# Optimization experiments

Measured on AMD Instinct MI355X. Metric: run time of the kernel, lower is better.

The kernel has to match this reference:

```python
import jax, jax.numpy as jnp
import numpy as np

TAG_THR = 0.1
MIN_HEIGHT = 0.0
PULL_WEIGHT = 1.0
PUSH_WEIGHT = 1.0
EPS = 1e-6


def _bbox_iou(boxes):
    # boxes: [N,4] -> IoU [N,N] (standard, no +1 offset; heights in the loss
    # are also computed without +1)
    x1, y1, x2, y2 = boxes[:, 0], boxes[:, 1], boxes[:, 2], boxes[:, 3]
    area = (x2 - x1) * (y2 - y1)
    iw = jnp.clip(jnp.minimum(x2[:, None], x2[None, :]) - jnp.maximum(x1[:, None], x1[None, :]), 0.0)
    ih = jnp.clip(jnp.minimum(y2[:, None], y2[None, :]) - jnp.maximum(y1[:, None], y1[None, :]), 0.0)
    inter = iw * ih
    union = area[:, None] + area[None, :] - inter
    return inter / jnp.maximum(union, 1e-12)


def _single_image(pred, gt_inds, proposals):
    # pred [N,D], gt_inds [N] int, proposals [N,5]
    N = pred.shape[0]
    heights = proposals[:, 3] - proposals[:, 1]
    valid = (gt_inds >= 0) & (heights > MIN_HEIGHT)
    scores = proposals[:, 4]
    iou = _bbox_iou(proposals[:, :4])  # [N,N]

    def step(state, _):
        alive, tot_pull, tot_push, pull_cnt, push_cnt = state
        active = jnp.sum(alive) >= 2  # pop i; if nothing remains, the torch loop breaks
        # i = highest-scoring remaining proposal (greedy, score-sorted)
        i = jnp.argmax(jnp.where(alive, scores, -jnp.inf))
        rem = alive.at[i].set(False)
        overlap = (iou[i] > 0.0) & rem
        diff = jnp.mean((pred - pred[i]) ** 2, axis=1)  # [N]
        check = diff < TAG_THR
        same = gt_inds == gt_inds[i]
        pull_m = overlap & same & ~check
        push_m = overlap & ~same & check
        pn = jnp.sum(pull_m)
        qn = jnp.sum(push_m)
        pull_l = jnp.sum(jnp.where(pull_m, diff * scores, 0.0)) / jnp.maximum(pn, 1).astype(diff.dtype)
        push_l = jnp.sum(jnp.where(push_m, jnp.exp(-diff) * scores, 0.0)) / jnp.maximum(qn, 1).astype(diff.dtype)
        add_pull = active & (pn > 0)
        add_push = active & (qn > 0)
        tot_pull = tot_pull + jnp.where(add_pull, pull_l, 0.0)
        tot_push = tot_push + jnp.where(add_push, push_l, 0.0)
        pull_cnt = pull_cnt + add_pull.astype(jnp.float32)
        push_cnt = push_cnt + add_push.astype(jnp.float32)
        # suppress everything overlapping i whose tag is already close (diff < thr)
        new_alive = rem & ~(overlap & check)
        alive = jnp.where(active, new_alive, alive)
        return (alive, tot_pull, tot_push, pull_cnt, push_cnt), None

    z = jnp.float32(0.0)
    init = (valid, z, z, z, z)
    (_, tot_pull, tot_push, pull_cnt, push_cnt), _ = jax.lax.scan(step, init, None, length=N)
    pull = tot_pull / (pull_cnt + EPS)
    push = tot_push / (push_cnt + EPS)
    return push, pull


def setup_inputs() -> dict:
    key = jax.random.key(0)
    k1, k2, k3, k4, k5, k6, k7 = jax.random.split(key, 7)
    IMGS, N, D = 4, 2000, 4
    pred = jax.random.normal(k1, (IMGS, N, D), dtype=jnp.float32)
    gt_inds = jax.random.randint(k2, (IMGS, N), 0, 50, dtype=jnp.int32)
    x1 = jax.random.uniform(k3, (IMGS, N), minval=0.0, maxval=800.0)
    y1 = jax.random.uniform(k4, (IMGS, N), minval=0.0, maxval=800.0)
    w = jax.random.uniform(k5, (IMGS, N), minval=8.0, maxval=128.0)
    h = jax.random.uniform(k6, (IMGS, N), minval=8.0, maxval=128.0)
    score = jax.random.uniform(k7, (IMGS, N), minval=0.0, maxval=1.0)
    proposals = jnp.stack([x1, y1, x1 + w, y1 + h, score], axis=-1).astype(jnp.float32)
    gt_bboxes = jax.random.uniform(jax.random.fold_in(key, 9), (IMGS, 20, 4), dtype=jnp.float32)
    return {"pred": pred, "gt_inds": gt_inds, "proposals": proposals, "gt_bboxes": gt_bboxes}


def reference(pred, gt_inds, proposals, gt_bboxes):
    # gt_bboxes is accepted by the torch forward but never used in the loss math.
    push, pull = jax.vmap(_single_image)(pred, gt_inds, proposals)  # per-image scalars
    img_num = pred.shape[0]
    push_loss = jnp.sum(push) / img_num * PUSH_WEIGHT
    pull_loss = jnp.sum(pull) / img_num * PULL_WEIGHT
    return push_loss, pull_loss
```

## Files before the change

kernel.cpp:

```cpp
#include <hip/hip_runtime.h>
#include <stdint.h>

#define BLOCK 256
#define KMAX 8
#define NWAVES (BLOCK / 64)
#define S2 2048
#define NW 32
#define NCH 32
#define SPB 16
#define PB (S2 / SPB)
#define RB (S2 / BLOCK)
#define PCAP 65536
#define LDSP2 4096
#define BCAP 64
#define EFF_INF 0x7FFFFFFF

__device__ inline int rank_of(const unsigned long long* ss, int j) {
    int jw = j >> 6, jb = j & 63;
    int rk = __popcll(ss[jw] & (jb ? (~0ull >> (64 - jb)) : 0ull));
    for (int w = 0; w < jw; ++w) rk += __popcll(ss[w]);
    return rk;
}

__global__ __launch_bounds__(BLOCK) void rankcount_kernel(
    const float* __restrict__ proposals,
    int* __restrict__ partial, int* __restrict__ pcnt, int N, int imgs)
{
    const int bi = blockIdx.x, bj = blockIdx.y, img = blockIdx.z;
    const int t = threadIdx.x;
    if (bi == 0 && bj == 0 && t == 0) pcnt[img] = 0;
    const float* P = proposals + (size_t)img * N * 5;
    __shared__ unsigned sj[BLOCK];
    const int jbase = bj * BLOCK;
    {
        int j = jbase + t;
        sj[t] = (j < N) ? __float_as_uint(P[j*5 + 4]) : 0u;
    }
    __syncthreads();
    const int i = bi * BLOCK + t;
    if (i >= N) return;
    const unsigned my = __float_as_uint(P[i*5 + 4]);
    int p = 0;
    const uint4* s4 = (const uint4*)sj;
#pragma unroll
    for (int q = 0; q < BLOCK/4; ++q) {
        uint4 v = s4[q];
        int jj = jbase + q*4;
        p += (int)((v.x > my) | ((v.x == my) & (jj + 0 < i)));
        p += (int)((v.y > my) | ((v.y == my) & (jj + 1 < i)));
        p += (int)((v.z > my) | ((v.z == my) & (jj + 2 < i)));
        p += (int)((v.w > my) | ((v.w == my) & (jj + 3 < i)));
    }
    partial[((size_t)(img*RB + bj))*S2 + i] = p;
}

__global__ __launch_bounds__(BLOCK) void rankscatter_kernel(
    const float* __restrict__ pred, const int* __restrict__ gt_inds,
    const float* __restrict__ proposals, const int* __restrict__ partial,
    float* __restrict__ soa, int* __restrict__ sgt, int N, int imgs)
{
    const int img = blockIdx.y, t = threadIdx.x;
    const int i = blockIdx.x * BLOCK + t;
    const size_t stride = (size_t)imgs * S2;
    const size_t base   = (size_t)img * S2;

    if (i >= N) {
        if (i < S2) {
#pragma unroll
            for (int a = 0; a < 9; ++a) soa[(size_t)a*stride + base + i] = 0.f;
            sgt[base + i] = -1;
        }
        return;
    }

    const float* P = proposals + (size_t)img * N * 5;
    const float* E = pred      + (size_t)img * N * 4;
    const int*   G = gt_inds   + (size_t)img * N;

    const float p0 = P[i*5+0], p1 = P[i*5+1], p2 = P[i*5+2],
                p3 = P[i*5+3], p4 = P[i*5+4];
    const float q0 = E[i*4+0], q1 = E[i*4+1], q2 = E[i*4+2], q3 = E[i*4+3];
    const int   gg = G[i];

    int p = 0;
#pragma unroll
    for (int b = 0; b < RB; ++b)
        p += partial[((size_t)(img*RB + b))*S2 + i];

    soa[0*stride + base + p] = p0;
    soa[1*stride + base + p] = p1;
    soa[2*stride + base + p] = p2;
    soa[3*stride + base + p] = p3;
    soa[4*stride + base + p] = p4;
    soa[5*stride + base + p] = q0;
    soa[6*stride + base + p] = q1;
    soa[7*stride + base + p] = q2;
    soa[8*stride + base + p] = q3;
    sgt[base + p] = gg;
}

__global__ __launch_bounds__(BLOCK) void suppairs_kernel(
    const float* __restrict__ soa, unsigned* __restrict__ pairs,
    int* __restrict__ pcnt, int N, int imgs)
{
    const int ic = blockIdx.x, jc = blockIdx.y, img = blockIdx.z;
    if (ic < jc) return;
    const int t = threadIdx.x, wave = t >> 6, lane = t & 63;
    const size_t stride = (size_t)imgs * S2, base = (size_t)img * S2;
    __shared__ float si[8][64];
    for (int idx = t; idx < 512; idx += BLOCK) {
        int f = idx >> 6, e = idx & 63;
        int a = (f < 4) ? f : f + 1;
        si[f][e] = soa[(size_t)a*stride + base + ic*64 + e];
    }
    __syncthreads();
    const int j = jc*64 + lane;
    const float jx1 = soa[0*stride+base+j], jy1 = soa[1*stride+base+j];
    const float jx2 = soa[2*stride+base+j], jy2 = soa[3*stride+base+j];
    const float j0  = soa[5*stride+base+j], j1  = soa[6*stride+base+j];
    const float j2  = soa[7*stride+base+j], j3  = soa[8*stride+base+j];
    const bool jin = (j < N);
    unsigned* PL = pairs + (size_t)img * PCAP;
    for (int ii = 0; ii < 16; ++ii) {
        int il = wave*16 + ii;
        int i  = ic*64 + il;
        float bx1 = si[0][il], by1 = si[1][il], bx2 = si[2][il], by2 = si[3][il];
        float f0  = si[4][il], f1  = si[5][il], f2  = si[6][il], f3  = si[7][il];
        bool s = false;
        if (jin && i < N && i > j) {
            float iw = fminf(jx2, bx2) - fmaxf(jx1, bx1);
            float ih = fminf(jy2, by2) - fmaxf(jy1, by1);
            if (iw > 0.f && ih > 0.f) {
                float d0 = j0-f0, d1 = j1-f1, d2 = j2-f2, d3 = j3-f3;
                float diff = 0.25f*(d0*d0 + d1*d1 + d2*d2 + d3*d3);
                s = diff < 0.1f;
            }
        }
        unsigned long long m = __ballot(s);
        if (m) {
            int leader = __ffsll((unsigned long long)m) - 1;
            int basei = 0;
            if (lane == leader) basei = atomicAdd(&pcnt[img], __popcll(m));
            basei = __shfl(basei, leader);
            if (s) {
                int idx = basei + __popcll(m & ((lane == 0) ? 0ull : (~0ull >> (64 - lane))));
                if (idx < PCAP) PL[idx] = ((unsigned)j << 11) | (unsigned)i;
            }
        }
    }
}

__global__ __launch_bounds__(64) void greedy_kernel(
    const unsigned* __restrict__ pairs, const int* __restrict__ pcnt,
    const int* __restrict__ sgt, const float* __restrict__ soa,
    unsigned long long* __restrict__ selw_out, int imgs)
{
    const int img = blockIdx.x, l = threadIdx.x;
    const size_t stride = (size_t)imgs * S2, base = (size_t)img * S2;
    __shared__ unsigned long long slocAll[S2];
    __shared__ unsigned spair[LDSP2];
    __shared__ unsigned bucket[NCH * BCAP];
    __shared__ int bcnt[NCH];
    __shared__ unsigned long long skilled[NW], ssel[NW];

    int P = pcnt[img]; if (P > PCAP) P = PCAP;
    const unsigned* PL = pairs + (size_t)img * PCAP;
    const bool staged = (P <= LDSP2);

    for (int x = l; x < S2; x += 64) slocAll[x] = 0ull;
    if (l < NCH) bcnt[l] = 0;
    if (staged) for (int p = l; p < P; p += 64) spair[p] = PL[p];

    for (int c = 0; c < NCH; ++c) {
        const int j = c*64 + l;
        int g = sgt[base + j];
        float a = soa[1*stride + base + j];
        float b = soa[3*stride + base + j];
        bool invalid = !(g >= 0 && (b - a) > 0.f);
        unsigned long long bb = __ballot(invalid);
        if (l == 0) skilled[c] = bb;
    }
    __syncthreads();

    for (int p = l; p < P; p += 64) {
        unsigned v = staged ? spair[p] : PL[p];
        int lo = v >> 11, hi = v & 2047;
        if ((lo >> 6) == (hi >> 6)) {
            atomicOr(&slocAll[hi], 1ull << (lo & 63));
        } else {
            int idx = atomicAdd(&bcnt[lo >> 6], 1);
            if (idx < BCAP) bucket[(lo >> 6)*BCAP + idx] = v;
        }
    }
    __syncthreads();

    const unsigned long long lowmask = (l == 0) ? 0ull : (~0ull >> (64 - l));

    for (int c = 0; c < NCH; ++c) {
        unsigned long long U = ~skilled[c];
        const unsigned long long loc = slocAll[c*64 + l];
        unsigned long long sel = 0ull;
        while (U) {
            bool inU = (U >> l) & 1ull;
            unsigned long long A = __ballot(inU && ((loc & U & lowmask) == 0ull));
            sel |= A;
            bool kill = inU && !((A >> l) & 1ull) && ((loc & A) != 0ull);
            unsigned long long K = __ballot(kill);
            U &= ~(A | K);
        }
        if (l == 0) ssel[c] = sel;
        if (sel != 0ull) {
            const int bc = bcnt[c];
            if (bc <= BCAP) {
                for (int q = l; q < bc; q += 64) {
                    unsigned v = bucket[c*BCAP + q];
                    int lo = v >> 11, hi = v & 2047;
                    if ((sel >> (lo & 63)) & 1ull)
                        atomicOr(&skilled[hi >> 6], 1ull << (hi & 63));
                }
            } else {
                for (int p = l; p < P; p += 64) {
                    unsigned v = PL[p];
                    int lo = v >> 11, hi = v & 2047;
                    if ((lo >> 6) == c && (hi >> 6) != c &&
                        ((sel >> (lo & 63)) & 1ull))
                        atomicOr(&skilled[hi >> 6], 1ull << (hi & 63));
                }
            }
        }
        __syncthreads();
    }
    if (l < NW) selw_out[(size_t)img*NW + l] = ssel[l];
}

__global__ __launch_bounds__(BLOCK) void effsteps_kernel(
    const unsigned* __restrict__ pairs, const int* __restrict__ pcnt,
    const unsigned long long* __restrict__ selw,
    const int* __restrict__ sgt, const float* __restrict__ soa,
    int* __restrict__ eff, int* __restrict__ nsteps, int imgs)
{
    const int img = blockIdx.x, t = threadIdx.x;
    const int lane = t & 63, wave = t >> 6;
    const size_t stride = (size_t)imgs * S2, base = (size_t)img * S2;
    __shared__ unsigned long long ss[NW];
    __shared__ int sistar[S2];
    __shared__ unsigned hist[S2];
    __shared__ int ints[2*NWAVES];
    __shared__ unsigned wsum[NWAVES];
    __shared__ int bm[NWAVES];
    if (t < NW) ss[t] = selw[(size_t)img*NW + t];
    for (int x = t; x < S2; x += BLOCK) { sistar[x] = EFF_INF; hist[x] = 0u; }
    __syncthreads();

    int P = pcnt[img]; if (P > PCAP) P = PCAP;
    const unsigned* PL = pairs + (size_t)img * PCAP;
    for (int p = t; p < P; p += BLOCK) {
        unsigned v = PL[p];
        int lo = v >> 11, hi = v & 2047;
        if ((ss[lo >> 6] >> (lo & 63)) & 1ull) atomicMin(&sistar[hi], lo);
    }
    __syncthreads();

    int myV = 0, mySc = 0;
#pragma unroll
    for (int k = 0; k < 8; ++k) {
        const int j = k*BLOCK + t;
        int g = sgt[base + j];
        float a = soa[1*stride+base+j], b = soa[3*stride+base+j];
        bool valid = (g >= 0) && ((b - a) > 0.f);
        bool selb  = (ss[j>>6] >> (j & 63)) & 1ull;
        int e;
        if (!valid) e = 0;
        else if (selb) { e = rank_of(ss, j); ++myV; ++mySc; }
        else {
            ++myV;
            int istar = sistar[j];
            if (istar == EFF_INF) e = EFF_INF;
            else { e = rank_of(ss, istar) + 1; atomicAdd(&hist[e - 1], 1u); }
        }
        eff[(size_t)img*S2 + j] = e;
    }
    __syncthreads();

    int v = myV, sc = mySc;
    for (int o = 32; o > 0; o >>= 1) { v += __shfl_down(v, o); sc += __shfl_down(sc, o); }
    if (lane == 0) { ints[wave] = v; ints[NWAVES + wave] = sc; }
    __syncthreads();
    int V = 0, Sc = 0;
    for (int w = 0; w < NWAVES; ++w) { V += ints[w]; Sc += ints[NWAVES + w]; }

    unsigned loc[8]; unsigned s = 0;
#pragma unroll
    for (int k = 0; k < 8; ++k) { s += hist[t*8 + k]; loc[k] = s; }
    unsigned tot = s;
    for (int o = 1; o < 64; o <<= 1) {
        unsigned u = __shfl_up(tot, o);
        if (lane >= o) tot += u;
    }
    if (lane == 63) wsum[wave] = tot;
    __syncthreads();
    unsigned woff = 0;
    for (int w = 0; w < wave; ++w) woff += wsum[w];
    unsigned exclP = woff + tot - s;
    __syncthreads();
#pragma unroll
    for (int k = 0; k < 8; ++k) hist[t*8 + k] = exclP + loc[k];
    __syncthreads();

    int best = EFF_INF;
    for (int r = t; r < Sc; r += BLOCK) {
        unsigned rem = (r == 0) ? 0u : hist[r - 1];
        int alive = V - r - (int)rem;
        if (alive < 2) best = min(best, r);
    }
    for (int o = 32; o > 0; o >>= 1) best = min(best, __shfl_down(best, o));
    if (lane == 0) bm[wave] = best;
    __syncthreads();
    if (t == 0) {
        int b = bm[0];
        for (int w = 1; w < NWAVES; ++w) b = min(b, bm[w]);
        nsteps[img] = min(b, Sc);
    }
}

__global__ __launch_bounds__(BLOCK) void pairs_kernel(
    const float* __restrict__ soa, const int* __restrict__ sgt,
    const int* __restrict__ eff, const unsigned long long* __restrict__ selw,
    const int* __restrict__ nsteps, float* __restrict__ partials, int imgs)
{
    const int ic = blockIdx.x, img = blockIdx.y;
    const int t = threadIdx.x, wave = t >> 6, lane = t & 63;
    const size_t stride = (size_t)imgs * S2, base = (size_t)img * S2;
    __shared__ unsigned long long ss[NW];
    __shared__ float pw[NWAVES][4];
    __shared__ int anyact;
    if (t < NW) ss[t] = selw[(size_t)img*NW + t];
    if (t == 0) anyact = 0;
    __syncthreads();
    const int ns = nsteps[img];

    float bx1[4], by1[4], bx2[4], by2[4], f0[4], f1[4], f2[4], f3[4];
    int bgt[4], rk[4]; bool act[4];
    bool any = false;
#pragma unroll
    for (int u = 0; u < 4; ++u) {
        const int i = ic*SPB + wave*4 + u;
        bool selb = (ss[i>>6] >> (i & 63)) & 1ull;
        int r = rank_of(ss, i);
        rk[u] = r;
        act[u] = selb && (r < ns);
        any |= act[u];
        if (act[u]) {
            bx1[u] = soa[0*stride+base+i]; by1[u] = soa[1*stride+base+i];
            bx2[u] = soa[2*stride+base+i]; by2[u] = soa[3*stride+base+i];
            f0[u]  = soa[5*stride+base+i]; f1[u]  = soa[6*stride+base+i];
            f2[u]  = soa[7*stride+base+i]; f3[u]  = soa[8*stride+base+i];
            bgt[u] = sgt[base + i];
        } else {
            bx1[u]=by1[u]=bx2[u]=by2[u]=0.f; f0[u]=f1[u]=f2[u]=f3[u]=0.f; bgt[u]=-2;
        }
    }
    if (any && lane == 0) anyact = 1;
    __syncthreads();
    if (!anyact) {
        if (t < 4) partials[((size_t)img*PB + ic)*4 + t] = 0.f;
        return;
    }

    float ps[4] = {0,0,0,0}, pn[4] = {0,0,0,0}, qs[4] = {0,0,0,0}, qn[4] = {0,0,0,0};
    for (int jt = 0; jt < NCH; ++jt) {
        const int j = jt*64 + lane;
        const float jx1 = soa[0*stride+base+j], jy1 = soa[1*stride+base+j];
        const float jx2 = soa[2*stride+base+j], jy2 = soa[3*stride+base+j];
        const float jsc = soa[4*stride+base+j];
        const float j0  = soa[5*stride+base+j], j1  = soa[6*stride+base+j];
        const float j2  = soa[7*stride+base+j], j3  = soa[8*stride+base+j];
        const int   jgt = sgt[base + j];
        const int   jef = eff[(size_t)img*S2 + j];
#pragma unroll
        for (int u = 0; u < 4; ++u) {
            if (!act[u]) continue;
            if (rk[u] < jef) {
                float iw = fminf(jx2, bx2[u]) - fmaxf(jx1, bx1[u]);
                float ih = fminf(jy2, by2[u]) - fmaxf(jy1, by1[u]);
                if (iw > 0.f && ih > 0.f) {
                    float d0 = j0 - f0[u], d1 = j1 - f1[u];
                    float d2 = j2 - f2[u], d3 = j3 - f3[u];
                    float diff = 0.25f*(d0*d0 + d1*d1 + d2*d2 + d3*d3);
                    bool check = diff < 0.1f;
                    bool same  = (jgt == bgt[u]);
                    if (same && !check)      { ps[u] += diff * jsc;       pn[u] += 1.f; }
                    else if (!same && check) { qs[u] += expf(-diff)*jsc;  qn[u] += 1.f; }
                }
            }
        }
    }

    float sPull = 0.f, cPull = 0.f, sPush = 0.f, cPush = 0.f;
#pragma unroll
    for (int u = 0; u < 4; ++u) {
        if (!act[u]) continue;
        float a0 = ps[u], a1 = pn[u], a2 = qs[u], a3 = qn[u];
        for (int o = 32; o > 0; o >>= 1) {
            a0 += __shfl_down(a0, o); a1 += __shfl_down(a1, o);
            a2 += __shfl_down(a2, o); a3 += __shfl_down(a3, o);
        }
        if (lane == 0) {
            if (a1 > 0.f) { sPull += a0 / a1; cPull += 1.f; }
            if (a3 > 0.f) { sPush += a2 / a3; cPush += 1.f; }
        }
    }
    if (lane == 0) {
        pw[wave][0] = sPull; pw[wave][1] = cPull;
        pw[wave][2] = sPush; pw[wave][3] = cPush;
    }
    __syncthreads();
    if (t == 0) {
        float a = 0, b = 0, c = 0, d = 0;
        for (int w = 0; w < NWAVES; ++w) {
            a += pw[w][0]; b += pw[w][1]; c += pw[w][2]; d += pw[w][3];
        }
        float* p = partials + ((size_t)img*PB + ic)*4;
        p[0] = a; p[1] = b; p[2] = c; p[3] = d;
    }
}

__global__ __launch_bounds__(BLOCK) void finalize_kernel(
    const float* __restrict__ partials, float* __restrict__ out, int imgs)
{
    const int t = threadIdx.x;
    __shared__ float a[8][4];
    if (t < 32) ((float*)a)[t] = 0.f;
    __syncthreads();
    for (int e = t; e < imgs * PB; e += BLOCK) {
        int img = e / PB;
        const float* p = partials + (size_t)e * 4;
#pragma unroll
        for (int k = 0; k < 4; ++k) {
            float v = p[k];
            if (v != 0.f) atomicAdd(&a[img][k], v);
        }
    }
    __syncthreads();
    if (t == 0) {
        float push = 0.f, pull = 0.f;
        for (int i = 0; i < imgs; ++i) {
            pull += a[i][0] / (a[i][1] + 1e-6f);
            push += a[i][2] / (a[i][3] + 1e-6f);
        }
        out[0] = push / (float)imgs;
        out[1] = pull / (float)imgs;
    }
}

__global__ __launch_bounds__(BLOCK) void tagloss_kernel(
    const float* __restrict__ pred, const int* __restrict__ gt_inds,
    const float* __restrict__ proposals, float* __restrict__ ws, int N)
{
    const int img = blockIdx.x, t = threadIdx.x;
    const int lane = t & 63, wav = t >> 6;
    const float* P = proposals + (size_t)img * N * 5;
    const float* E = pred      + (size_t)img * N * 4;
    const int*   G = gt_inds   + (size_t)img * N;
    float x1[KMAX], y1[KMAX], x2[KMAX], y2[KMAX], sc[KMAX];
    float e0[KMAX], e1[KMAX], e2[KMAX], e3[KMAX];
    int gt[KMAX]; unsigned amask = 0u; int local_alive = 0;
#pragma unroll
    for (int k = 0; k < KMAX; ++k) {
        int j = k * BLOCK + t;
        if (j < N) {
            x1[k]=P[j*5+0]; y1[k]=P[j*5+1]; x2[k]=P[j*5+2]; y2[k]=P[j*5+3]; sc[k]=P[j*5+4];
            e0[k]=E[j*4+0]; e1[k]=E[j*4+1]; e2[k]=E[j*4+2]; e3[k]=E[j*4+3]; gt[k]=G[j];
            if (gt[k] >= 0 && (y2[k]-y1[k]) > 0.0f) { amask |= 1u<<k; local_alive++; }
        } else { x1[k]=y1[k]=x2[k]=y2[k]=0.f; sc[k]=0.f; e0[k]=e1[k]=e2[k]=e3[k]=0.f; gt[k]=-1; }
    }
    __shared__ unsigned long long s_key[NWAVES];
    __shared__ float s_b[9];
    __shared__ float s_part[NWAVES][5];
    int alive_count;
    {
        float v = (float)local_alive;
#pragma unroll
        for (int o = 32; o > 0; o >>= 1) v += __shfl_down(v, o);
        if (lane == 0) s_part[wav][0] = v;
        __syncthreads();
        float tot = 0.f;
        for (int w = 0; w < NWAVES; ++w) tot += s_part[w][0];
        alive_count = (int)tot;
    }
    float tot_pull=0.f, tot_push=0.f, pull_cnt=0.f, push_cnt=0.f;
    while (alive_count >= 2) {
        unsigned long long key = 0ull;
#pragma unroll
        for (int k = 0; k < KMAX; ++k)
            if (amask & (1u<<k)) {
                unsigned long long kk = ((unsigned long long)__float_as_uint(sc[k])<<32)
                                      | (unsigned long long)(0xFFFFFFFFu - (unsigned)(k*BLOCK+t));
                if (kk > key) key = kk;
            }
#pragma unroll
        for (int o = 32; o > 0; o >>= 1) {
            unsigned long long ok = __shfl_down(key, o);
            if (ok > key) key = ok;
        }
        if (lane == 0) s_key[wav] = key;
        __syncthreads();
        unsigned long long bk = s_key[0];
        for (int w = 1; w < NWAVES; ++w) if (s_key[w] > bk) bk = s_key[w];
        const int i = (int)(0xFFFFFFFFu - (unsigned)(bk & 0xFFFFFFFFull));
        if ((i & (BLOCK-1)) == t) {
            int k = i / BLOCK;
            s_b[0]=x1[k]; s_b[1]=y1[k]; s_b[2]=x2[k]; s_b[3]=y2[k];
            s_b[4]=e0[k]; s_b[5]=e1[k]; s_b[6]=e2[k]; s_b[7]=e3[k];
            s_b[8]=__int_as_float(gt[k]);
        }
        __syncthreads();
        const float bx1=s_b[0], by1=s_b[1], bx2=s_b[2], by2=s_b[3];
        const float f0=s_b[4], f1=s_b[5], f2=s_b[6], f3=s_b[7];
        const int bgt = __float_as_int(s_b[8]);
        const float areai = (bx2-bx1)*(by2-by1);
        float psum=0.f,qsum=0.f,pn=0.f,qn=0.f,scnt=0.f;
#pragma unroll
        for (int k = 0; k < KMAX; ++k) {
            if (!(amask & (1u<<k))) continue;
            int j = k*BLOCK+t;
            if (j == i) { amask &= ~(1u<<k); continue; }
            float iw = fmaxf(fminf(x2[k],bx2)-fmaxf(x1[k],bx1),0.f);
            float ih = fmaxf(fminf(y2[k],by2)-fmaxf(y1[k],by1),0.f);
            float inter = iw*ih;
            float uni = (x2[k]-x1[k])*(y2[k]-y1[k]) + areai - inter;
            float iou = inter / fmaxf(uni, 1e-12f);
            if (iou > 0.f) {
                float d0=e0[k]-f0,d1=e1[k]-f1,d2=e2[k]-f2,d3=e3[k]-f3;
                float diff = 0.25f*(d0*d0+d1*d1+d2*d2+d3*d3);
                bool check = diff < 0.1f;
                bool same = (gt[k]==bgt);
                if (same && !check) { psum += diff*sc[k]; pn += 1.f; }
                if (!same && check) { qsum += __expf(-diff)*sc[k]; qn += 1.f; }
                if (check)          { amask &= ~(1u<<k); scnt += 1.f; }
            }
        }
        float r0=psum,r1=pn,r2=qsum,r3=qn,r4=scnt;
#pragma unroll
        for (int o = 32; o > 0; o >>= 1) {
            r0+=__shfl_down(r0,o); r1+=__shfl_down(r1,o); r2+=__shfl_down(r2,o);
            r3+=__shfl_down(r3,o); r4+=__shfl_down(r4,o);
        }
        if (lane == 0) { s_part[wav][0]=r0;s_part[wav][1]=r1;s_part[wav][2]=r2;s_part[wav][3]=r3;s_part[wav][4]=r4; }
        __syncthreads();
        float T0=0,T1=0,T2=0,T3=0,T4=0;
        for (int w = 0; w < NWAVES; ++w) {
            T0+=s_part[w][0];T1+=s_part[w][1];T2+=s_part[w][2];T3+=s_part[w][3];T4+=s_part[w][4];
        }
        if (T1 > 0.f) { tot_pull += T0/T1; pull_cnt += 1.f; }
        if (T3 > 0.f) { tot_push += T2/T3; push_cnt += 1.f; }
        alive_count -= 1 + (int)T4;
    }
    if (t == 0) {
        ws[img*2+0] = tot_push / (push_cnt + 1e-6f);
        ws[img*2+1] = tot_pull / (pull_cnt + 1e-6f);
    }
}

__global__ void finalize_fb_kernel(const float* __restrict__ ws,
                                   float* __restrict__ out, int imgs)
{
    if (threadIdx.x == 0 && blockIdx.x == 0) {
        float push = 0.f, pull = 0.f;
        for (int k = 0; k < imgs; ++k) { push += ws[2*k]; pull += ws[2*k+1]; }
        out[0] = push / (float)imgs;
        out[1] = pull / (float)imgs;
    }
}

extern "C" void kernel_launch(void* const* d_in, const int* in_sizes, int n_in,
                              void* d_out, int out_size, void* d_ws, size_t ws_size,
                              hipStream_t stream) {
    const float* pred      = (const float*)d_in[0];
    const int*   gt_inds   = (const int*)  d_in[1];
    const float* proposals = (const float*)d_in[2];
    const int imgs = in_sizes[3] / 80;
    const int N    = in_sizes[1] / imgs;

    size_t off = 0;
    auto alloc = [&](size_t b) { size_t o = off; off += (b + 255) & ~(size_t)255; return o; };
    const size_t soa_off  = alloc((size_t)9 * imgs * S2 * 4);
    const size_t sgt_off  = alloc((size_t)imgs * S2 * 4);
    const size_t sel_off  = alloc((size_t)imgs * NW * 8);
    const size_t eff_off  = alloc((size_t)imgs * S2 * 4);
    const size_t nst_off  = alloc((size_t)imgs * 4);
    const size_t par_off  = alloc((size_t)imgs * PB * 16);
    const size_t rnk_off  = alloc((size_t)imgs * RB * S2 * 4);
    const size_t prs_off  = alloc((size_t)imgs * PCAP * 4);
    const size_t pcn_off  = alloc((size_t)imgs * 4);
    const size_t need = off;

    if (N <= S2 && imgs <= 8 && ws_size >= need) {
        char* w = (char*)d_ws;
        float*              soa  = (float*)(w + soa_off);
        int*                sgt  = (int*)(w + sgt_off);
        unsigned long long* sel  = (unsigned long long*)(w + sel_off);
        int*                eff  = (int*)(w + eff_off);
        int*                nst  = (int*)(w + nst_off);
        float*              par  = (float*)(w + par_off);
        int*                rnk  = (int*)(w + rnk_off);
        unsigned*           prs  = (unsigned*)(w + prs_off);
        int*                pcn  = (int*)(w + pcn_off);

        rankcount_kernel<<<dim3(RB, RB, imgs), BLOCK, 0, stream>>>(
            proposals, rnk, pcn, N, imgs);
        rankscatter_kernel<<<dim3(RB, imgs), BLOCK, 0, stream>>>(
            pred, gt_inds, proposals, rnk, soa, sgt, N, imgs);
        suppairs_kernel<<<dim3(NCH, NCH, imgs), BLOCK, 0, stream>>>(
            soa, prs, pcn, N, imgs);
        greedy_kernel<<<imgs, 64, 0, stream>>>(prs, pcn, sgt, soa, sel, imgs);
        effsteps_kernel<<<imgs, BLOCK, 0, stream>>>(prs, pcn, sel, sgt, soa,
                                                    eff, nst, imgs);
        pairs_kernel<<<dim3(PB, imgs), BLOCK, 0, stream>>>(soa, sgt, eff, sel,
                                                           nst, par, imgs);
        finalize_kernel<<<1, BLOCK, 0, stream>>>(par, (float*)d_out, imgs);
    } else {
        float* ws = (float*)d_ws;
        tagloss_kernel<<<imgs, BLOCK, 0, stream>>>(pred, gt_inds, proposals, ws, N);
        finalize_fb_kernel<<<1, 64, 0, stream>>>(ws, (float*)d_out, imgs);
    }
}
```

Measured before the change: 152.1 us.

## Fuse greedy with effsteps and pairs with finalize to cut kernel launches

```diff
diff --git a/kernel.cpp b/kernel.cpp
--- a/kernel.cpp
+++ b/kernel.cpp
@@ -15,20 +15,18 @@
 #define BCAP 64
 #define EFF_INF 0x7FFFFFFF
 
-__device__ inline int rank_of(const unsigned long long* ss, int j) {
-    int jw = j >> 6, jb = j & 63;
-    int rk = __popcll(ss[jw] & (jb ? (~0ull >> (64 - jb)) : 0ull));
-    for (int w = 0; w < jw; ++w) rk += __popcll(ss[w]);
-    return rk;
-}
-
 __global__ __launch_bounds__(BLOCK) void rankcount_kernel(
     const float* __restrict__ proposals,
-    int* __restrict__ partial, int* __restrict__ pcnt, int N, int imgs)
+    int* __restrict__ partial, int* __restrict__ pcnt,
+    float* __restrict__ acc, int* __restrict__ done, int N, int imgs)
 {
     const int bi = blockIdx.x, bj = blockIdx.y, img = blockIdx.z;
     const int t = threadIdx.x;
-    if (bi == 0 && bj == 0 && t == 0) pcnt[img] = 0;
+    if (bi == 0 && bj == 0 && img == 0) {
+        if (t < imgs) pcnt[t] = 0;
+        if (t >= 64 && t < 64 + imgs*4) acc[t - 64] = 0.f;
+        if (t == 128) *done = 0;
+    }
     const float* P = proposals + (size_t)img * N * 5;
     __shared__ unsigned sj[BLOCK];
     const int jbase = bj * BLOCK;
@@ -124,14 +122,13 @@
     for (int ii = 0; ii < 16; ++ii) {
         int il = wave*16 + ii;
         int i  = ic*64 + il;
-        float bx1 = si[0][il], by1 = si[1][il], bx2 = si[2][il], by2 = si[3][il];
-        float f0  = si[4][il], f1  = si[5][il], f2  = si[6][il], f3  = si[7][il];
         bool s = false;
         if (jin && i < N && i > j) {
-            float iw = fminf(jx2, bx2) - fmaxf(jx1, bx1);
-            float ih = fminf(jy2, by2) - fmaxf(jy1, by1);
+            float iw = fminf(jx2, si[2][il]) - fmaxf(jx1, si[0][il]);
+            float ih = fminf(jy2, si[3][il]) - fmaxf(jy1, si[1][il]);
             if (iw > 0.f && ih > 0.f) {
-                float d0 = j0-f0, d1 = j1-f1, d2 = j2-f2, d3 = j3-f3;
+                float d0 = j0-si[4][il], d1 = j1-si[5][il];
+                float d2 = j2-si[6][il], d3 = j3-si[7][il];
                 float diff = 0.25f*(d0*d0 + d1*d1 + d2*d2 + d3*d3);
                 s = diff < 0.1f;
             }
@@ -150,39 +147,52 @@
     }
 }
 
-__global__ __launch_bounds__(64) void greedy_kernel(
+__global__ __launch_bounds__(BLOCK) void greedyeff_kernel(
     const unsigned* __restrict__ pairs, const int* __restrict__ pcnt,
     const int* __restrict__ sgt, const float* __restrict__ soa,
-    unsigned long long* __restrict__ selw_out, int imgs)
+    unsigned long long* __restrict__ selw, int* __restrict__ eff,
+    int* __restrict__ nsteps, int imgs)
 {
-    const int img = blockIdx.x, l = threadIdx.x;
+    const int img = blockIdx.x, t = threadIdx.x;
+    const int lane = t & 63, wave = t >> 6;
     const size_t stride = (size_t)imgs * S2, base = (size_t)img * S2;
-    __shared__ unsigned long long slocAll[S2];
+
+    __shared__ __align__(16) char A[16384];
     __shared__ unsigned spair[LDSP2];
     __shared__ unsigned bucket[NCH * BCAP];
     __shared__ int bcnt[NCH];
-    __shared__ unsigned long long skilled[NW], ssel[NW];
+    __shared__ unsigned long long skilled[NW], ssel[NW], svalid[NW];
+    __shared__ int pfx[NW + 1];
+    __shared__ unsigned wsum[NWAVES];
+    __shared__ int bm[NWAVES];
+    __shared__ int sV;
+
+    unsigned long long* slocAll = (unsigned long long*)A;
 
     int P = pcnt[img]; if (P > PCAP) P = PCAP;
     const unsigned* PL = pairs + (size_t)img * PCAP;
     const bool staged = (P <= LDSP2);
 
-    for (int x = l; x < S2; x += 64) slocAll[x] = 0ull;
-    if (l < NCH) bcnt[l] = 0;
-    if (staged) for (int p = l; p < P; p += 64) spair[p] = PL[p];
-
-    for (int c = 0; c < NCH; ++c) {
-        const int j = c*64 + l;
-        int g = sgt[base + j];
+    for (int x = t; x < S2; x += BLOCK) slocAll[x] = 0ull;
+    if (t < NCH) bcnt[t] = 0;
+    if (t == 0) sV = 0;
+    __syncthreads();
+    if (staged) for (int p = t; p < P; p += BLOCK) spair[p] = PL[p];
+    for (int g = wave; g < NCH; g += NWAVES) {
+        int j = g*64 + lane;
+        int gv = sgt[base + j];
         float a = soa[1*stride + base + j];
         float b = soa[3*stride + base + j];
-        bool invalid = !(g >= 0 && (b - a) > 0.f);
+        bool invalid = !(gv >= 0 && (b - a) > 0.f);
         unsigned long long bb = __ballot(invalid);
-        if (l == 0) skilled[c] = bb;
-    }
-    __syncthreads();
-
-    for (int p = l; p < P; p += 64) {
+        if (lane == 0) {
+            skilled[g] = bb;
+            svalid[g] = ~bb;
+            atomicAdd(&sV, 64 - __popcll(bb));
+        }
+    }
+    __syncthreads();
+    for (int p = t; p < P; p += BLOCK) {
         unsigned v = staged ? spair[p] : PL[p];
         int lo = v >> 11, hi = v & 2047;
         if ((lo >> 6) == (hi >> 6)) {
@@ -194,104 +204,87 @@
     }
     __syncthreads();
 
-    const unsigned long long lowmask = (l == 0) ? 0ull : (~0ull >> (64 - l));
-
-    for (int c = 0; c < NCH; ++c) {
-        unsigned long long U = ~skilled[c];
-        const unsigned long long loc = slocAll[c*64 + l];
-        unsigned long long sel = 0ull;
-        while (U) {
-            bool inU = (U >> l) & 1ull;
-            unsigned long long A = __ballot(inU && ((loc & U & lowmask) == 0ull));
-            sel |= A;
-            bool kill = inU && !((A >> l) & 1ull) && ((loc & A) != 0ull);
-            unsigned long long K = __ballot(kill);
-            U &= ~(A | K);
-        }
-        if (l == 0) ssel[c] = sel;
-        if (sel != 0ull) {
-            const int bc = bcnt[c];
-            if (bc <= BCAP) {
-                for (int q = l; q < bc; q += 64) {
-                    unsigned v = bucket[c*BCAP + q];
-                    int lo = v >> 11, hi = v & 2047;
-                    if ((sel >> (lo & 63)) & 1ull)
-                        atomicOr(&skilled[hi >> 6], 1ull << (hi & 63));
+    if (wave == 0) {
+        const unsigned long long lowmask = (lane == 0) ? 0ull : (~0ull >> (64 - lane));
+        for (int c = 0; c < NCH; ++c) {
+            unsigned long long U = ~skilled[c];
+            const unsigned long long loc = slocAll[c*64 + lane];
+            unsigned long long sel = 0ull;
+            while (U) {
+                bool inU = (U >> lane) & 1ull;
+                unsigned long long Am = __ballot(inU && ((loc & U & lowmask) == 0ull));
+                sel |= Am;
+                bool kill = inU && !((Am >> lane) & 1ull) && ((loc & Am) != 0ull);
+                unsigned long long K = __ballot(kill);
+                U &= ~(Am | K);
+            }
+            if (lane == 0) ssel[c] = sel;
+            if (sel != 0ull) {
+                const int bc = bcnt[c];
+                if (bc <= BCAP) {
+                    for (int q = lane; q < bc; q += 64) {
+                        unsigned v = bucket[c*BCAP + q];
+                        int lo = v >> 11, hi = v & 2047;
+                        if ((sel >> (lo & 63)) & 1ull)
+                            atomicOr(&skilled[hi >> 6], 1ull << (hi & 63));
+                    }
+                } else {
+                    for (int p = lane; p < P; p += 64) {
+                        unsigned v = PL[p];
+                        int lo = v >> 11, hi = v & 2047;
+                        if ((lo >> 6) == c && (hi >> 6) != c &&
+                            ((sel >> (lo & 63)) & 1ull))
+                            atomicOr(&skilled[hi >> 6], 1ull << (hi & 63));
+                    }
                 }
-            } else {
-                for (int p = l; p < P; p += 64) {
-                    unsigned v = PL[p];
-                    int lo = v >> 11, hi = v & 2047;
-                    if ((lo >> 6) == c && (hi >> 6) != c &&
-                        ((sel >> (lo & 63)) & 1ull))
-                        atomicOr(&skilled[hi >> 6], 1ull << (hi & 63));
-                }
-            }
-        }
-        __syncthreads();
-    }
-    if (l < NW) selw_out[(size_t)img*NW + l] = ssel[l];
-}
-
-__global__ __launch_bounds__(BLOCK) void effsteps_kernel(
-    const unsigned* __restrict__ pairs, const int* __restrict__ pcnt,
-    const unsigned long long* __restrict__ selw,
-    const int* __restrict__ sgt, const float* __restrict__ soa,
-    int* __restrict__ eff, int* __restrict__ nsteps, int imgs)
-{
-    const int img = blockIdx.x, t = threadIdx.x;
-    const int lane = t & 63, wave = t >> 6;
-    const size_t stride = (size_t)imgs * S2, base = (size_t)img * S2;
-    __shared__ unsigned long long ss[NW];
-    __shared__ int sistar[S2];
-    __shared__ unsigned hist[S2];
-    __shared__ int ints[2*NWAVES];
-    __shared__ unsigned wsum[NWAVES];
-    __shared__ int bm[NWAVES];
-    if (t < NW) ss[t] = selw[(size_t)img*NW + t];
+            }
+        }
+    }
+    __syncthreads();
+    if (t < NW) selw[(size_t)img*NW + t] = ssel[t];
+
+    int* sistar = (int*)A;
+    unsigned* hist = (unsigned*)(A + 8192);
     for (int x = t; x < S2; x += BLOCK) { sistar[x] = EFF_INF; hist[x] = 0u; }
-    __syncthreads();
-
-    int P = pcnt[img]; if (P > PCAP) P = PCAP;
-    const unsigned* PL = pairs + (size_t)img * PCAP;
+    if (t == 0) {
+        int s = 0;
+        for (int w = 0; w < NW; ++w) { pfx[w] = s; s += __popcll(ssel[w]); }
+        pfx[NW] = s;
+    }
+    __syncthreads();
     for (int p = t; p < P; p += BLOCK) {
-        unsigned v = PL[p];
+        unsigned v = staged ? spair[p] : PL[p];
         int lo = v >> 11, hi = v & 2047;
-        if ((ss[lo >> 6] >> (lo & 63)) & 1ull) atomicMin(&sistar[hi], lo);
-    }
-    __syncthreads();
-
-    int myV = 0, mySc = 0;
+        if ((ssel[lo >> 6] >> (lo & 63)) & 1ull) atomicMin(&sistar[hi], lo);
+    }
+    __syncthreads();
 #pragma unroll
     for (int k = 0; k < 8; ++k) {
         const int j = k*BLOCK + t;
-        int g = sgt[base + j];
-        float a = soa[1*stride+base+j], b = soa[3*stride+base+j];
-        bool valid = (g >= 0) && ((b - a) > 0.f);
-        bool selb  = (ss[j>>6] >> (j & 63)) & 1ull;
+        const int jw = j >> 6, jb = j & 63;
+        bool valid = (svalid[jw] >> jb) & 1ull;
+        bool selb  = (ssel[jw] >> jb) & 1ull;
         int e;
         if (!valid) e = 0;
-        else if (selb) { e = rank_of(ss, j); ++myV; ++mySc; }
+        else if (selb)
+            e = pfx[jw] + __popcll(ssel[jw] & (jb ? (~0ull >> (64 - jb)) : 0ull));
         else {
-            ++myV;
-            int istar = sistar[j];
-            if (istar == EFF_INF) e = EFF_INF;
-            else { e = rank_of(ss, istar) + 1; atomicAdd(&hist[e - 1], 1u); }
+            int is = sistar[j];
+            if (is == EFF_INF) e = EFF_INF;
+            else {
+                int iw_ = is >> 6, ib = is & 63;
+                e = pfx[iw_] + __popcll(ssel[iw_] & (ib ? (~0ull >> (64 - ib)) : 0ull)) + 1;
+                atomicAdd(&hist[e - 1], 1u);
+            }
         }
         eff[(size_t)img*S2 + j] = e;
     }
     __syncthreads();
 
-    int v = myV, sc = mySc;
-    for (int o = 32; o > 0; o >>= 1) { v += __shfl_down(v, o); sc += __shfl_down(sc, o); }
-    if (lane == 0) { ints[wave] = v; ints[NWAVES + wave] = sc; }
-    __syncthreads();
-    int V = 0, Sc = 0;
-    for (int w = 0; w < NWAVES; ++w) { V += ints[w]; Sc += ints[NWAVES + w]; }
-
-    unsigned loc[8]; unsigned s = 0;
-#pragma unroll
-    for (int k = 0; k < 8; ++k) { s += hist[t*8 + k]; loc[k] = s; }
+    const int V = sV, Sc = pfx[NW];
+    unsigned loc8[8]; unsigned s = 0;
+#pragma unroll
+    for (int k = 0; k < 8; ++k) { s += hist[t*8 + k]; loc8[k] = s; }
     unsigned tot = s;
     for (int o = 1; o < 64; o <<= 1) {
         unsigned u = __shfl_up(tot, o);
@@ -304,9 +297,8 @@
     unsigned exclP = woff + tot - s;
     __syncthreads();
 #pragma unroll
-    for (int k = 0; k < 8; ++k) hist[t*8 + k] = exclP + loc[k];
-    __syncthreads();
-
+    for (int k = 0; k < 8; ++k) hist[t*8 + k] = exclP + loc8[k];
+    __syncthreads();
     int best = EFF_INF;
     for (int r = t; r < Sc; r += BLOCK) {
         unsigned rem = (r == 0) ? 0u : hist[r - 1];
@@ -323,17 +315,18 @@
     }
 }
 
-__global__ __launch_bounds__(BLOCK) void pairs_kernel(
+__global__ __launch_bounds__(BLOCK) void pairsfinal_kernel(
     const float* __restrict__ soa, const int* __restrict__ sgt,
     const int* __restrict__ eff, const unsigned long long* __restrict__ selw,
-    const int* __restrict__ nsteps, float* __restrict__ partials, int imgs)
+    const int* __restrict__ nsteps, float* __restrict__ acc,
+    int* __restrict__ done, float* __restrict__ out, int imgs)
 {
     const int ic = blockIdx.x, img = blockIdx.y;
     const int t = threadIdx.x, wave = t >> 6, lane = t & 63;
     const size_t stride = (size_t)imgs * S2, base = (size_t)img * S2;
     __shared__ unsigned long long ss[NW];
     __shared__ float pw[NWAVES][4];
-    __shared__ int anyact;
+    __shared__ int anyact, ticket;
     if (t < NW) ss[t] = selw[(size_t)img*NW + t];
     if (t == 0) anyact = 0;
     __syncthreads();
@@ -345,8 +338,10 @@
 #pragma unroll
     for (int u = 0; u < 4; ++u) {
         const int i = ic*SPB + wave*4 + u;
-        bool selb = (ss[i>>6] >> (i & 63)) & 1ull;
-        int r = rank_of(ss, i);
+        const int iw_ = i >> 6, ib = i & 63;
+        bool selb = (ss[iw_] >> ib) & 1ull;
+        int r = __popcll(ss[iw_] & (ib ? (~0ull >> (64 - ib)) : 0ull));
+        for (int w = 0; w < iw_; ++w) r += __popcll(ss[w]);
         rk[u] = r;
         act[u] = selb && (r < ns);
         any |= act[u];
@@ -362,91 +357,78 @@
     }
     if (any && lane == 0) anyact = 1;
     __syncthreads();
-    if (!anyact) {
-        if (t < 4) partials[((size_t)img*PB + ic)*4 + t] = 0.f;
-        return;
-    }
-
-    float ps[4] = {0,0,0,0}, pn[4] = {0,0,0,0}, qs[4] = {0,0,0,0}, qn[4] = {0,0,0,0};
-    for (int jt = 0; jt < NCH; ++jt) {
-        const int j = jt*64 + lane;
-        const float jx1 = soa[0*stride+base+j], jy1 = soa[1*stride+base+j];
-        const float jx2 = soa[2*stride+base+j], jy2 = soa[3*stride+base+j];
-        const float jsc = soa[4*stride+base+j];
-        const float j0  = soa[5*stride+base+j], j1  = soa[6*stride+base+j];
-        const float j2  = soa[7*stride+base+j], j3  = soa[8*stride+base+j];
-        const int   jgt = sgt[base + j];
-        const int   jef = eff[(size_t)img*S2 + j];
+
+    if (anyact) {
+        float ps[4] = {0,0,0,0}, pn[4] = {0,0,0,0};
+        float qs[4] = {0,0,0,0}, qn[4] = {0,0,0,0};
+        for (int jt = 0; jt < NCH; ++jt) {
+            const int j = jt*64 + lane;
+            const float jx1 = soa[0*stride+base+j], jy1 = soa[1*stride+base+j];
+            const float jx2 = soa[2*stride+base+j], jy2 = soa[3*stride+base+j];
+            const float jsc = soa[4*stride+base+j];
+            const float j0  = soa[5*stride+base+j], j1  = soa[6*stride+base+j];
+            const float j2  = soa[7*stride+base+j], j3  = soa[8*stride+base+j];
+            const int   jgt = sgt[base + j];
+            const int   jef = eff[(size_t)img*S2 + j];
+#pragma unroll
+            for (int u = 0; u < 4; ++u) {
+                if (!act[u]) continue;
+                if (rk[u] < jef) {
+                    float iw = fminf(jx2, bx2[u]) - fmaxf(jx1, bx1[u]);
+                    float ih = fminf(jy2, by2[u]) - fmaxf(jy1, by1[u]);
+                    if (iw > 0.f && ih > 0.f) {
+                        float d0 = j0 - f0[u], d1 = j1 - f1[u];
+                        float d2 = j2 - f2[u], d3 = j3 - f3[u];
+                        float diff = 0.25f*(d0*d0 + d1*d1 + d2*d2 + d3*d3);
+                        bool check = diff < 0.1f;
+                        bool same  = (jgt == bgt[u]);
+                        if (same && !check)      { ps[u] += diff * jsc;       pn[u] += 1.f; }
+                        else if (!same && check) { qs[u] += expf(-diff)*jsc;  qn[u] += 1.f; }
+                    }
+                }
+            }
+        }
+        float sPull = 0.f, cPull = 0.f, sPush = 0.f, cPush = 0.f;
 #pragma unroll
         for (int u = 0; u < 4; ++u) {
             if (!act[u]) continue;
-            if (rk[u] < jef) {
-                float iw = fminf(jx2, bx2[u]) - fmaxf(jx1, bx1[u]);
-                float ih = fminf(jy2, by2[u]) - fmaxf(jy1, by1[u]);
-                if (iw > 0.f && ih > 0.f) {
-                    float d0 = j0 - f0[u], d1 = j1 - f1[u];
-                    float d2 = j2 - f2[u], d3 = j3 - f3[u];
-                    float diff = 0.25f*(d0*d0 + d1*d1 + d2*d2 + d3*d3);
-                    bool check = diff < 0.1f;
-                    bool same  = (jgt == bgt[u]);
-                    if (same && !check)      { ps[u] += diff * jsc;       pn[u] += 1.f; }
-                    else if (!same && check) { qs[u] += expf(-diff)*jsc;  qn[u] += 1.f; }
-                }
-            }
-        }
-    }
-
-    float sPull = 0.f, cPull = 0.f, sPush = 0.f, cPush = 0.f;
-#pragma unroll
-    for (int u = 0; u < 4; ++u) {
-        if (!act[u]) continue;
-        float a0 = ps[u], a1 = pn[u], a2 = qs[u], a3 = qn[u];
-        for (int o = 32; o > 0; o >>= 1) {
-            a0 += __shfl_down(a0, o); a1 += __shfl_down(a1, o);
-            a2 += __shfl_down(a2, o); a3 += __shfl_down(a3, o);
+            float a0 = ps[u], a1 = pn[u], a2 = qs[u], a3 = qn[u];
+            for (int o = 32; o > 0; o >>= 1) {
+                a0 += __shfl_down(a0, o); a1 += __shfl_down(a1, o);
+                a2 += __shfl_down(a2, o); a3 += __shfl_down(a3, o);
+            }
+            if (lane == 0) {
+                if (a1 > 0.f) { sPull += a0 / a1; cPull += 1.f; }
+                if (a3 > 0.f) { sPush += a2 / a3; cPush += 1.f; }
+            }
         }
         if (lane == 0) {
-            if (a1 > 0.f) { sPull += a0 / a1; cPull += 1.f; }
-            if (a3 > 0.f) { sPush += a2 / a3; cPush += 1.f; }
-        }
-    }
-    if (lane == 0) {
-        pw[wave][0] = sPull; pw[wave][1] = cPull;
-        pw[wave][2] = sPush; pw[wave][3] = cPush;
-    }
-    __syncthreads();
-    if (t == 0) {
-        float a = 0, b = 0, c = 0, d = 0;
-        for (int w = 0; w < NWAVES; ++w) {
-            a += pw[w][0]; b += pw[w][1]; c += pw[w][2]; d += pw[w][3];
-        }
-        float* p = partials + ((size_t)img*PB + ic)*4;
-        p[0] = a; p[1] = b; p[2] = c; p[3] = d;
-    }
-}
-
-__global__ __launch_bounds__(BLOCK) void finalize_kernel(
-    const float* __restrict__ partials, float* __restrict__ out, int imgs)
-{
-    const int t = threadIdx.x;
-    __shared__ float a[8][4];
-    if (t < 32) ((float*)a)[t] = 0.f;
-    __syncthreads();
-    for (int e = t; e < imgs * PB; e += BLOCK) {
-        int img = e / PB;
-        const float* p = partials + (size_t)e * 4;
-#pragma unroll
-        for (int k = 0; k < 4; ++k) {
-            float v = p[k];
-            if (v != 0.f) atomicAdd(&a[img][k], v);
-        }
-    }
-    __syncthreads();
-    if (t == 0) {
+            pw[wave][0] = sPull; pw[wave][1] = cPull;
+            pw[wave][2] = sPush; pw[wave][3] = cPush;
+        }
+        __syncthreads();
+        if (t == 0) {
+            float a = 0, b = 0, c = 0, d = 0;
+            for (int w = 0; w < NWAVES; ++w) {
+                a += pw[w][0]; b += pw[w][1]; c += pw[w][2]; d += pw[w][3];
+            }
+            if (a != 0.f) atomicAdd(&acc[img*4+0], a);
+            if (b != 0.f) atomicAdd(&acc[img*4+1], b);
+            if (c != 0.f) atomicAdd(&acc[img*4+2], c);
+            if (d != 0.f) atomicAdd(&acc[img*4+3], d);
+        }
+    }
+
+    __syncthreads();
+    __threadfence();
+    if (t == 0) ticket = atomicAdd(done, 1);
+    __syncthreads();
+    if (ticket == PB * imgs - 1 && t == 0) {
+        __threadfence();
         float push = 0.f, pull = 0.f;
         for (int i = 0; i < imgs; ++i) {
-            pull += a[i][0] / (a[i][1] + 1e-6f);
-            push += a[i][2] / (a[i][3] + 1e-6f);
+            pull += acc[i*4+0] / (acc[i*4+1] + 1e-6f);
+            push += acc[i*4+2] / (acc[i*4+3] + 1e-6f);
         }
         out[0] = push / (float)imgs;
         out[1] = pull / (float)imgs;
@@ -589,10 +571,11 @@
     const size_t sel_off  = alloc((size_t)imgs * NW * 8);
     const size_t eff_off  = alloc((size_t)imgs * S2 * 4);
     const size_t nst_off  = alloc((size_t)imgs * 4);
-    const size_t par_off  = alloc((size_t)imgs * PB * 16);
     const size_t rnk_off  = alloc((size_t)imgs * RB * S2 * 4);
     const size_t prs_off  = alloc((size_t)imgs * PCAP * 4);
     const size_t pcn_off  = alloc((size_t)imgs * 4);
+    const size_t acc_off  = alloc((size_t)imgs * 16);
+    const size_t don_off  = alloc(4);
     const size_t need = off;
 
     if (N <= S2 && imgs <= 8 && ws_size >= need) {
@@ -602,23 +585,22 @@
         unsigned long long* sel  = (unsigned long long*)(w + sel_off);
         int*                eff  = (int*)(w + eff_off);
         int*                nst  = (int*)(w + nst_off);
-        float*              par  = (float*)(w + par_off);
         int*                rnk  = (int*)(w + rnk_off);
         unsigned*           prs  = (unsigned*)(w + prs_off);
         int*                pcn  = (int*)(w + pcn_off);
+        float*              acc  = (float*)(w + acc_off);
+        int*                don  = (int*)(w + don_off);
 
         rankcount_kernel<<<dim3(RB, RB, imgs), BLOCK, 0, stream>>>(
-            proposals, rnk, pcn, N, imgs);
+            proposals, rnk, pcn, acc, don, N, imgs);
         rankscatter_kernel<<<dim3(RB, imgs), BLOCK, 0, stream>>>(
             pred, gt_inds, proposals, rnk, soa, sgt, N, imgs);
         suppairs_kernel<<<dim3(NCH, NCH, imgs), BLOCK, 0, stream>>>(
             soa, prs, pcn, N, imgs);
-        greedy_kernel<<<imgs, 64, 0, stream>>>(prs, pcn, sgt, soa, sel, imgs);
-        effsteps_kernel<<<imgs, BLOCK, 0, stream>>>(prs, pcn, sel, sgt, soa,
-                                                    eff, nst, imgs);
-        pairs_kernel<<<dim3(PB, imgs), BLOCK, 0, stream>>>(soa, sgt, eff, sel,
-                                                           nst, par, imgs);
-        finalize_kernel<<<1, BLOCK, 0, stream>>>(par, (float*)d_out, imgs);
+        greedyeff_kernel<<<imgs, BLOCK, 0, stream>>>(prs, pcn, sgt, soa,
+                                                     sel, eff, nst, imgs);
+        pairsfinal_kernel<<<dim3(PB, imgs), BLOCK, 0, stream>>>(
+            soa, sgt, eff, sel, nst, acc, don, (float*)d_out, imgs);
     } else {
         float* ws = (float*)d_ws;
         tagloss_kernel<<<imgs, BLOCK, 0, stream>>>(pred, gt_inds, proposals, ws, N);
```

New measurement: 152.5 us. Within noise of the previous version (+0.3%).
